# Kernel optimization log

Hardware: AMD Instinct MI355X
Metric: run time of the kernel (lower is better)

## Reference

```python
import jax, jax.numpy as jnp
import numpy as np

N, C_IN, C_RED, H, W = 16, 256, 64, 48, 48


def conv1x1(x, w, b):
    # x: [N, Cin, H, W], w: [Cout, Cin], b: [Cout]
    return jnp.einsum('nchw,oc->nohw', x, w) + b[None, :, None, None]


def setup_inputs() -> dict:
    key = jax.random.key(0)
    ks = jax.random.split(key, 10)
    s_in = 1.0 / np.sqrt(C_IN)
    s_red = 1.0 / np.sqrt(C_RED)
    return {
        'feature_maps': jax.random.normal(ks[0], (N, C_IN, H, W), jnp.float32),
        'global_channel_output': jax.random.normal(ks[1], (N, C_IN, H, W), jnp.float32),
        'Wq': jax.random.uniform(ks[2], (C_RED, C_IN), jnp.float32, -s_in, s_in),
        'bq': jax.random.uniform(ks[3], (C_RED,), jnp.float32, -s_in, s_in),
        'Wk': jax.random.uniform(ks[4], (C_RED, C_IN), jnp.float32, -s_in, s_in),
        'bk': jax.random.uniform(ks[5], (C_RED,), jnp.float32, -s_in, s_in),
        'Wv': jax.random.uniform(ks[6], (C_RED, C_IN), jnp.float32, -s_in, s_in),
        'bv': jax.random.uniform(ks[7], (C_RED,), jnp.float32, -s_in, s_in),
        'Watt': jax.random.uniform(ks[8], (C_IN, C_RED), jnp.float32, -s_red, s_red),
        'batt': jax.random.uniform(ks[9], (C_IN,), jnp.float32, -s_red, s_red),
    }


def reference(feature_maps, global_channel_output, Wq, bq, Wk, bk, Wv, bv, Watt, batt):
    n, _, h, w = feature_maps.shape
    hw = h * w
    q = conv1x1(feature_maps, Wq, bq).reshape(n, -1, hw)   # [N, Cr, HW]
    k = conv1x1(feature_maps, Wk, bk).reshape(n, -1, hw)   # [N, Cr, HW]
    v = conv1x1(feature_maps, Wv, bv).reshape(n, -1, hw)   # [N, Cr, HW]
    # key^T @ query -> [N, HW, HW]
    qk = jnp.einsum('nci,ncj->nij', k, q)
    # global (flattened) softmax over the whole HWxHW matrix per batch element
    qk = jax.nn.softmax(qk.reshape(n, hw * hw), axis=-1).reshape(n, hw, hw)
    att = jnp.einsum('nci,nij->ncj', v, qk).reshape(n, -1, h, w)  # [N, Cr, H, W]
    att = conv1x1(att, Watt, batt)                                 # [N, Cin, H, W]
    return global_channel_output * att + global_channel_output
```

## Files before the change

### kernel.cpp

```cpp
#include <hip/hip_runtime.h>
#include <hip/hip_bf16.h>
#include <stdint.h>

#define NB   16
#define CIN  256
#define CRED 64
#define HW   2304
#define NJT  36

typedef __bf16 bf16;
typedef __bf16 bf16x8 __attribute__((ext_vector_type(8)));
typedef __bf16 bf16x4 __attribute__((ext_vector_type(4)));
typedef float  f32x4  __attribute__((ext_vector_type(4)));

__global__ __launch_bounds__(256) void qkv_kernel(
    const float* __restrict__ x,
    const float* __restrict__ Wq, const float* __restrict__ bq,
    const float* __restrict__ Wk, const float* __restrict__ bk,
    const float* __restrict__ Wv, const float* __restrict__ bv,
    bf16* __restrict__ qT, bf16* __restrict__ kT, bf16* __restrict__ v)
{
    __shared__ __align__(16) bf16 sX[64 * 264];
    const int jt = blockIdx.x, n = blockIdx.y;
    const int jbase = jt * 64;
    const int tid = threadIdx.x;
    const int lane = tid & 63, w = tid >> 6;
    const int l15 = lane & 15, q4 = lane >> 4;

    const float* xn = x + ((size_t)n * CIN) * HW + jbase;
    #pragma unroll
    for (int it = 0; it < 16; ++it) {
        int idx = tid + 256 * it;
        int c = idx >> 4, p4 = idx & 15;
        const float4 vv = *(const float4*)(xn + c * HW + p4 * 4);
        sX[(p4 * 4 + 0) * 264 + c] = (bf16)vv.x;
        sX[(p4 * 4 + 1) * 264 + c] = (bf16)vv.y;
        sX[(p4 * 4 + 2) * 264 + c] = (bf16)vv.z;
        sX[(p4 * 4 + 3) * 264 + c] = (bf16)vv.w;
    }
    __syncthreads();

    const float* Ws[3] = {Wq, Wk, Wv};
    const float* bs[3] = {bq, bk, bv};
    #pragma unroll
    for (int wi = 0; wi < 3; ++wi) {
        bf16x8 a[8];
        const float* Wp = Ws[wi] + (w * 16 + l15) * CIN + q4 * 8;
        #pragma unroll
        for (int ks = 0; ks < 8; ++ks) {
            float4 f0 = *(const float4*)(Wp + ks * 32);
            float4 f1 = *(const float4*)(Wp + ks * 32 + 4);
            bf16x8 t = {(bf16)f0.x, (bf16)f0.y, (bf16)f0.z, (bf16)f0.w,
                        (bf16)f1.x, (bf16)f1.y, (bf16)f1.z, (bf16)f1.w};
            a[ks] = t;
        }
        f32x4 acc[4] = {};
        #pragma unroll
        for (int nt = 0; nt < 4; ++nt) {
            #pragma unroll
            for (int ks = 0; ks < 8; ++ks) {
                bf16x8 b = *(const bf16x8*)(sX + (nt * 16 + l15) * 264 + ks * 32 + q4 * 8);
                acc[nt] = __builtin_amdgcn_mfma_f32_16x16x32_bf16(a[ks], b, acc[nt], 0, 0, 0);
            }
        }
        const int crb = w * 16 + q4 * 4;
        const float b0 = bs[wi][crb], b1 = bs[wi][crb + 1],
                    b2 = bs[wi][crb + 2], b3 = bs[wi][crb + 3];
        if (wi < 2) {
            bf16* dst = (wi == 0 ? qT : kT) + ((size_t)n * HW) * 64;
            #pragma unroll
            for (int nt = 0; nt < 4; ++nt) {
                int pos = jbase + nt * 16 + l15;
                bf16x4 pk = {(bf16)(acc[nt].x + b0), (bf16)(acc[nt].y + b1),
                             (bf16)(acc[nt].z + b2), (bf16)(acc[nt].w + b3)};
                *(bf16x4*)(dst + pos * 64 + crb) = pk;
            }
        } else {
            bf16* dst = v + ((size_t)n * CRED) * HW;
            #pragma unroll
            for (int nt = 0; nt < 4; ++nt) {
                int pos = jbase + nt * 16 + l15;
                dst[(crb + 0) * HW + pos] = (bf16)(acc[nt].x + b0);
                dst[(crb + 1) * HW + pos] = (bf16)(acc[nt].y + b1);
                dst[(crb + 2) * HW + pos] = (bf16)(acc[nt].z + b2);
                dst[(crb + 3) * HW + pos] = (bf16)(acc[nt].w + b3);
            }
        }
    }
}

__global__ __launch_bounds__(256) void attn_kernel(
    const bf16* __restrict__ qT, const bf16* __restrict__ kT,
    const bf16* __restrict__ v,
    float* __restrict__ OT, float* __restrict__ Z)
{
    __shared__ __align__(16) bf16 sQ[64 * 72];
    __shared__ __align__(16) bf16 sK[64 * 72];
    __shared__ __align__(16) bf16 sV[64 * 72];
    __shared__ __align__(16) bf16 sP[64 * 72];
    const int jt = blockIdx.x, n = blockIdx.y;
    const int jbase = jt * 64;
    const int tid = threadIdx.x;
    const int lane = tid & 63, w = tid >> 6;
    const int l15 = lane & 15, q4 = lane >> 4;

    {
        const uint4* src = (const uint4*)(qT + ((size_t)n * HW + jbase) * 64);
        uint4* dst = (uint4*)sQ;
        for (int i = tid; i < 512; i += 256) {
            int r = i >> 3, c = i & 7;
            dst[r * 9 + c] = src[r * 8 + c];
        }
    }
    f32x4 oacc[4] = {};
    float zacc = 0.f;
    const uint4* ksrc = (const uint4*)(kT + ((size_t)n * HW) * 64);
    const bf16* vbase = v + ((size_t)n * CRED) * HW;

    for (int ib = 0; ib < NJT; ++ib) {
        const int ibase = ib * 64;
        __syncthreads();
        {
            uint4* dk = (uint4*)sK;
            uint4* dv = (uint4*)sV;
            const uint4* sk = ksrc + ibase * 8;
            for (int i = tid; i < 512; i += 256) {
                int r = i >> 3, c = i & 7;
                dk[r * 9 + c] = sk[r * 8 + c];
                dv[r * 9 + c] = *(const uint4*)(vbase + r * HW + ibase + c * 8);
            }
        }
        __syncthreads();
        f32x4 s[4];
        #pragma unroll
        for (int nt = 0; nt < 4; ++nt) {
            f32x4 accs = {};
            #pragma unroll
            for (int ks = 0; ks < 2; ++ks) {
                bf16x8 afr = *(const bf16x8*)(sK + (w * 16 + l15) * 72 + ks * 32 + q4 * 8);
                bf16x8 bfr = *(const bf16x8*)(sQ + (nt * 16 + l15) * 72 + ks * 32 + q4 * 8);
                accs = __builtin_amdgcn_mfma_f32_16x16x32_bf16(afr, bfr, accs, 0, 0, 0);
            }
            s[nt] = accs;
        }
        #pragma unroll
        for (int nt = 0; nt < 4; ++nt) {
            float p0 = __expf(s[nt].x), p1 = __expf(s[nt].y);
            float p2 = __expf(s[nt].z), p3 = __expf(s[nt].w);
            zacc += (p0 + p1) + (p2 + p3);
            bf16x4 pk = {(bf16)p0, (bf16)p1, (bf16)p2, (bf16)p3};
            *(bf16x4*)(sP + (nt * 16 + l15) * 72 + w * 16 + q4 * 4) = pk;
        }
        __syncthreads();
        #pragma unroll
        for (int nt = 0; nt < 4; ++nt) {
            #pragma unroll
            for (int ks = 0; ks < 2; ++ks) {
                bf16x8 afr = *(const bf16x8*)(sV + (w * 16 + l15) * 72 + ks * 32 + q4 * 8);
                bf16x8 bfr = *(const bf16x8*)(sP + (nt * 16 + l15) * 72 + ks * 32 + q4 * 8);
                oacc[nt] = __builtin_amdgcn_mfma_f32_16x16x32_bf16(afr, bfr, oacc[nt], 0, 0, 0);
            }
        }
    }
    float* OTn = OT + ((size_t)n * HW) * 64;
    #pragma unroll
    for (int nt = 0; nt < 4; ++nt) {
        int pos = jbase + nt * 16 + l15;
        *(f32x4*)(OTn + pos * 64 + w * 16 + q4 * 4) = oacc[nt];
    }
    #pragma unroll
    for (int off = 32; off > 0; off >>= 1) zacc += __shfl_down(zacc, off);
    if (lane == 0) atomicAdd(Z + n, zacc);
}

__global__ __launch_bounds__(256) void out_kernel(
    const float* __restrict__ OT, const float* __restrict__ Z,
    const float* __restrict__ Watt, const float* __restrict__ batt,
    const float* __restrict__ g, float* __restrict__ out)
{
    __shared__ __align__(16) bf16 sO[64 * 72];
    const int jt = blockIdx.x, n = blockIdx.y;
    const int jbase = jt * 64;
    const int tid = threadIdx.x;
    const int lane = tid & 63, w = tid >> 6;
    const int l15 = lane & 15, q4 = lane >> 4;
    const float invZ = 1.0f / Z[n];

    const float* On = OT + ((size_t)n * HW + jbase) * 64;
    for (int i = tid; i < 1024; i += 256) {
        int r = i >> 4, c4 = i & 15;
        float4 vv = *(const float4*)(On + r * 64 + c4 * 4);
        bf16x4 pk = {(bf16)(vv.x * invZ), (bf16)(vv.y * invZ),
                     (bf16)(vv.z * invZ), (bf16)(vv.w * invZ)};
        *(bf16x4*)(sO + r * 72 + c4 * 4) = pk;
    }
    __syncthreads();

    bf16x8 a[4][2];
    #pragma unroll
    for (int mt = 0; mt < 4; ++mt) {
        const float* Wp = Watt + (w * 64 + mt * 16 + l15) * 64 + q4 * 8;
        #pragma unroll
        for (int ks = 0; ks < 2; ++ks) {
            float4 f0 = *(const float4*)(Wp + ks * 32);
            float4 f1 = *(const float4*)(Wp + ks * 32 + 4);
            bf16x8 t = {(bf16)f0.x, (bf16)f0.y, (bf16)f0.z, (bf16)f0.w,
                        (bf16)f1.x, (bf16)f1.y, (bf16)f1.z, (bf16)f1.w};
            a[mt][ks] = t;
        }
    }
    const float* gp = g + ((size_t)n * CIN) * HW;
    float* op = out + ((size_t)n * CIN) * HW;
    #pragma unroll
    for (int mt = 0; mt < 4; ++mt) {
        #pragma unroll
        for (int nt = 0; nt < 4; ++nt) {
            f32x4 acc = {};
            #pragma unroll
            for (int ks = 0; ks < 2; ++ks) {
                bf16x8 b = *(const bf16x8*)(sO + (nt * 16 + l15) * 72 + ks * 32 + q4 * 8);
                acc = __builtin_amdgcn_mfma_f32_16x16x32_bf16(a[mt][ks], b, acc, 0, 0, 0);
            }
            const int co = w * 64 + mt * 16 + q4 * 4;
            const int pos = jbase + nt * 16 + l15;
            const float b0 = batt[co], b1 = batt[co + 1], b2 = batt[co + 2], b3 = batt[co + 3];
            const float g0 = gp[(co + 0) * HW + pos], g1 = gp[(co + 1) * HW + pos];
            const float g2 = gp[(co + 2) * HW + pos], g3 = gp[(co + 3) * HW + pos];
            op[(co + 0) * HW + pos] = g0 * (acc.x + b0 + 1.0f);
            op[(co + 1) * HW + pos] = g1 * (acc.y + b1 + 1.0f);
            op[(co + 2) * HW + pos] = g2 * (acc.z + b2 + 1.0f);
            op[(co + 3) * HW + pos] = g3 * (acc.w + b3 + 1.0f);
        }
    }
}

extern "C" void kernel_launch(void* const* d_in, const int* in_sizes, int n_in,
                              void* d_out, int out_size, void* d_ws, size_t ws_size,
                              hipStream_t stream) {
    const float* x    = (const float*)d_in[0];
    const float* g    = (const float*)d_in[1];
    const float* Wq   = (const float*)d_in[2];
    const float* bq   = (const float*)d_in[3];
    const float* Wk   = (const float*)d_in[4];
    const float* bk   = (const float*)d_in[5];
    const float* Wv   = (const float*)d_in[6];
    const float* bv   = (const float*)d_in[7];
    const float* Watt = (const float*)d_in[8];
    const float* batt = (const float*)d_in[9];
    float* out = (float*)d_out;

    char* ws = (char*)d_ws;
    const size_t qkv_sz = (size_t)NB * HW * CRED * sizeof(bf16);
    bf16*  qT = (bf16*)(ws);
    bf16*  kT = (bf16*)(ws + qkv_sz);
    bf16*  vv = (bf16*)(ws + 2 * qkv_sz);
    float* OT = (float*)(ws + 3 * qkv_sz);
    float* Z  = (float*)(ws + 3 * qkv_sz + (size_t)NB * HW * CRED * sizeof(float));

    hipMemsetAsync(Z, 0, NB * sizeof(float), stream);

    dim3 grid(NJT, NB), blk(256);
    qkv_kernel<<<grid, blk, 0, stream>>>(x, Wq, bq, Wk, bk, Wv, bv, qT, kT, vv);
    attn_kernel<<<grid, blk, 0, stream>>>(qT, kT, vv, OT, Z);
    out_kernel<<<grid, blk, 0, stream>>>(OT, Z, Watt, batt, g, out);
}
```

Baseline: 255.0 us.

## Split attention key range across blocks and reduce partials in output kernel

```diff
diff --git a/kernel.cpp b/kernel.cpp
--- a/kernel.cpp
+++ b/kernel.cpp
@@ -7,6 +7,8 @@
 #define CRED 64
 #define HW   2304
 #define NJT  36
+#define NIG  4
+#define NIT  9
 
 typedef __bf16 bf16;
 typedef __bf16 bf16x8 __attribute__((ext_vector_type(8)));
@@ -92,13 +94,13 @@
 __global__ __launch_bounds__(256) void attn_kernel(
     const bf16* __restrict__ qT, const bf16* __restrict__ kT,
     const bf16* __restrict__ v,
-    float* __restrict__ OT, float* __restrict__ Z)
+    float* __restrict__ OTp, float* __restrict__ Z)
 {
     __shared__ __align__(16) bf16 sQ[64 * 72];
     __shared__ __align__(16) bf16 sK[64 * 72];
     __shared__ __align__(16) bf16 sV[64 * 72];
     __shared__ __align__(16) bf16 sP[64 * 72];
-    const int jt = blockIdx.x, n = blockIdx.y;
+    const int jt = blockIdx.x, ig = blockIdx.y, n = blockIdx.z;
     const int jbase = jt * 64;
     const int tid = threadIdx.x;
     const int lane = tid & 63, w = tid >> 6;
@@ -112,13 +114,21 @@
             dst[r * 9 + c] = src[r * 8 + c];
         }
     }
+    __syncthreads();
+    bf16x8 qf[4][2];
+    #pragma unroll
+    for (int nt = 0; nt < 4; ++nt)
+        #pragma unroll
+        for (int ks = 0; ks < 2; ++ks)
+            qf[nt][ks] = *(const bf16x8*)(sQ + (nt * 16 + l15) * 72 + ks * 32 + q4 * 8);
+
     f32x4 oacc[4] = {};
     float zacc = 0.f;
     const uint4* ksrc = (const uint4*)(kT + ((size_t)n * HW) * 64);
     const bf16* vbase = v + ((size_t)n * CRED) * HW;
 
-    for (int ib = 0; ib < NJT; ++ib) {
-        const int ibase = ib * 64;
+    for (int it = 0; it < NIT; ++it) {
+        const int ibase = (ig * NIT + it) * 64;
         __syncthreads();
         {
             uint4* dk = (uint4*)sK;
@@ -131,38 +141,31 @@
             }
         }
         __syncthreads();
-        f32x4 s[4];
+        bf16x8 kf0 = *(const bf16x8*)(sK + (w * 16 + l15) * 72 + 0 * 32 + q4 * 8);
+        bf16x8 kf1 = *(const bf16x8*)(sK + (w * 16 + l15) * 72 + 1 * 32 + q4 * 8);
         #pragma unroll
         for (int nt = 0; nt < 4; ++nt) {
             f32x4 accs = {};
-            #pragma unroll
-            for (int ks = 0; ks < 2; ++ks) {
-                bf16x8 afr = *(const bf16x8*)(sK + (w * 16 + l15) * 72 + ks * 32 + q4 * 8);
-                bf16x8 bfr = *(const bf16x8*)(sQ + (nt * 16 + l15) * 72 + ks * 32 + q4 * 8);
-                accs = __builtin_amdgcn_mfma_f32_16x16x32_bf16(afr, bfr, accs, 0, 0, 0);
-            }
-            s[nt] = accs;
-        }
-        #pragma unroll
-        for (int nt = 0; nt < 4; ++nt) {
-            float p0 = __expf(s[nt].x), p1 = __expf(s[nt].y);
-            float p2 = __expf(s[nt].z), p3 = __expf(s[nt].w);
+            accs = __builtin_amdgcn_mfma_f32_16x16x32_bf16(kf0, qf[nt][0], accs, 0, 0, 0);
+            accs = __builtin_amdgcn_mfma_f32_16x16x32_bf16(kf1, qf[nt][1], accs, 0, 0, 0);
+            float p0 = __expf(accs.x), p1 = __expf(accs.y);
+            float p2 = __expf(accs.z), p3 = __expf(accs.w);
             zacc += (p0 + p1) + (p2 + p3);
             bf16x4 pk = {(bf16)p0, (bf16)p1, (bf16)p2, (bf16)p3};
             *(bf16x4*)(sP + (nt * 16 + l15) * 72 + w * 16 + q4 * 4) = pk;
         }
         __syncthreads();
+        bf16x8 vf0 = *(const bf16x8*)(sV + (w * 16 + l15) * 72 + 0 * 32 + q4 * 8);
+        bf16x8 vf1 = *(const bf16x8*)(sV + (w * 16 + l15) * 72 + 1 * 32 + q4 * 8);
         #pragma unroll
         for (int nt = 0; nt < 4; ++nt) {
-            #pragma unroll
-            for (int ks = 0; ks < 2; ++ks) {
-                bf16x8 afr = *(const bf16x8*)(sV + (w * 16 + l15) * 72 + ks * 32 + q4 * 8);
-                bf16x8 bfr = *(const bf16x8*)(sP + (nt * 16 + l15) * 72 + ks * 32 + q4 * 8);
-                oacc[nt] = __builtin_amdgcn_mfma_f32_16x16x32_bf16(afr, bfr, oacc[nt], 0, 0, 0);
-            }
-        }
-    }
-    float* OTn = OT + ((size_t)n * HW) * 64;
+            bf16x8 p0 = *(const bf16x8*)(sP + (nt * 16 + l15) * 72 + 0 * 32 + q4 * 8);
+            bf16x8 p1 = *(const bf16x8*)(sP + (nt * 16 + l15) * 72 + 1 * 32 + q4 * 8);
+            oacc[nt] = __builtin_amdgcn_mfma_f32_16x16x32_bf16(vf0, p0, oacc[nt], 0, 0, 0);
+            oacc[nt] = __builtin_amdgcn_mfma_f32_16x16x32_bf16(vf1, p1, oacc[nt], 0, 0, 0);
+        }
+    }
+    float* OTn = OTp + (((size_t)ig * NB + n) * HW) * 64;
     #pragma unroll
     for (int nt = 0; nt < 4; ++nt) {
         int pos = jbase + nt * 16 + l15;
@@ -174,63 +177,60 @@
 }
 
 __global__ __launch_bounds__(256) void out_kernel(
-    const float* __restrict__ OT, const float* __restrict__ Z,
+    const float* __restrict__ OTp, const float* __restrict__ Z,
     const float* __restrict__ Watt, const float* __restrict__ batt,
     const float* __restrict__ g, float* __restrict__ out)
 {
-    __shared__ __align__(16) bf16 sO[64 * 72];
+    __shared__ __align__(16) bf16 sO[16 * 72];
     const int jt = blockIdx.x, n = blockIdx.y;
-    const int jbase = jt * 64;
+    const int jbase = jt * 16;
     const int tid = threadIdx.x;
     const int lane = tid & 63, w = tid >> 6;
     const int l15 = lane & 15, q4 = lane >> 4;
     const float invZ = 1.0f / Z[n];
 
-    const float* On = OT + ((size_t)n * HW + jbase) * 64;
-    for (int i = tid; i < 1024; i += 256) {
-        int r = i >> 4, c4 = i & 15;
-        float4 vv = *(const float4*)(On + r * 64 + c4 * 4);
-        bf16x4 pk = {(bf16)(vv.x * invZ), (bf16)(vv.y * invZ),
-                     (bf16)(vv.z * invZ), (bf16)(vv.w * invZ)};
+    {
+        int r = tid >> 4, c4 = tid & 15;
+        const float* p = OTp + (((size_t)n * HW) + jbase + r) * 64 + c4 * 4;
+        float4 v0 = *(const float4*)(p);
+        float4 v1 = *(const float4*)(p + (size_t)NB * HW * 64);
+        float4 v2 = *(const float4*)(p + 2 * (size_t)NB * HW * 64);
+        float4 v3 = *(const float4*)(p + 3 * (size_t)NB * HW * 64);
+        bf16x4 pk = {(bf16)((v0.x + v1.x + v2.x + v3.x) * invZ),
+                     (bf16)((v0.y + v1.y + v2.y + v3.y) * invZ),
+                     (bf16)((v0.z + v1.z + v2.z + v3.z) * invZ),
+                     (bf16)((v0.w + v1.w + v2.w + v3.w) * invZ)};
         *(bf16x4*)(sO + r * 72 + c4 * 4) = pk;
     }
     __syncthreads();
 
-    bf16x8 a[4][2];
+    const float* gp = g + ((size_t)n * CIN) * HW;
+    float* op = out + ((size_t)n * CIN) * HW;
+    bf16x8 b0 = *(const bf16x8*)(sO + l15 * 72 + 0 * 32 + q4 * 8);
+    bf16x8 b1 = *(const bf16x8*)(sO + l15 * 72 + 1 * 32 + q4 * 8);
     #pragma unroll
     for (int mt = 0; mt < 4; ++mt) {
         const float* Wp = Watt + (w * 64 + mt * 16 + l15) * 64 + q4 * 8;
-        #pragma unroll
-        for (int ks = 0; ks < 2; ++ks) {
-            float4 f0 = *(const float4*)(Wp + ks * 32);
-            float4 f1 = *(const float4*)(Wp + ks * 32 + 4);
-            bf16x8 t = {(bf16)f0.x, (bf16)f0.y, (bf16)f0.z, (bf16)f0.w,
-                        (bf16)f1.x, (bf16)f1.y, (bf16)f1.z, (bf16)f1.w};
-            a[mt][ks] = t;
-        }
-    }
-    const float* gp = g + ((size_t)n * CIN) * HW;
-    float* op = out + ((size_t)n * CIN) * HW;
-    #pragma unroll
-    for (int mt = 0; mt < 4; ++mt) {
-        #pragma unroll
-        for (int nt = 0; nt < 4; ++nt) {
-            f32x4 acc = {};
-            #pragma unroll
-            for (int ks = 0; ks < 2; ++ks) {
-                bf16x8 b = *(const bf16x8*)(sO + (nt * 16 + l15) * 72 + ks * 32 + q4 * 8);
-                acc = __builtin_amdgcn_mfma_f32_16x16x32_bf16(a[mt][ks], b, acc, 0, 0, 0);
-            }
-            const int co = w * 64 + mt * 16 + q4 * 4;
-            const int pos = jbase + nt * 16 + l15;
-            const float b0 = batt[co], b1 = batt[co + 1], b2 = batt[co + 2], b3 = batt[co + 3];
-            const float g0 = gp[(co + 0) * HW + pos], g1 = gp[(co + 1) * HW + pos];
-            const float g2 = gp[(co + 2) * HW + pos], g3 = gp[(co + 3) * HW + pos];
-            op[(co + 0) * HW + pos] = g0 * (acc.x + b0 + 1.0f);
-            op[(co + 1) * HW + pos] = g1 * (acc.y + b1 + 1.0f);
-            op[(co + 2) * HW + pos] = g2 * (acc.z + b2 + 1.0f);
-            op[(co + 3) * HW + pos] = g3 * (acc.w + b3 + 1.0f);
-        }
+        float4 f0 = *(const float4*)(Wp);
+        float4 f1 = *(const float4*)(Wp + 4);
+        float4 f2 = *(const float4*)(Wp + 32);
+        float4 f3 = *(const float4*)(Wp + 36);
+        bf16x8 a0 = {(bf16)f0.x, (bf16)f0.y, (bf16)f0.z, (bf16)f0.w,
+                     (bf16)f1.x, (bf16)f1.y, (bf16)f1.z, (bf16)f1.w};
+        bf16x8 a1 = {(bf16)f2.x, (bf16)f2.y, (bf16)f2.z, (bf16)f2.w,
+                     (bf16)f3.x, (bf16)f3.y, (bf16)f3.z, (bf16)f3.w};
+        f32x4 acc = {};
+        acc = __builtin_amdgcn_mfma_f32_16x16x32_bf16(a0, b0, acc, 0, 0, 0);
+        acc = __builtin_amdgcn_mfma_f32_16x16x32_bf16(a1, b1, acc, 0, 0, 0);
+        const int co = w * 64 + mt * 16 + q4 * 4;
+        const int pos = jbase + l15;
+        const float c0 = batt[co], c1 = batt[co + 1], c2 = batt[co + 2], c3 = batt[co + 3];
+        const float g0 = gp[(co + 0) * HW + pos], g1 = gp[(co + 1) * HW + pos];
+        const float g2 = gp[(co + 2) * HW + pos], g3 = gp[(co + 3) * HW + pos];
+        op[(co + 0) * HW + pos] = g0 * (acc.x + c0 + 1.0f);
+        op[(co + 1) * HW + pos] = g1 * (acc.y + c1 + 1.0f);
+        op[(co + 2) * HW + pos] = g2 * (acc.z + c2 + 1.0f);
+        op[(co + 3) * HW + pos] = g3 * (acc.w + c3 + 1.0f);
     }
 }
 
@@ -254,13 +254,13 @@
     bf16*  qT = (bf16*)(ws);
     bf16*  kT = (bf16*)(ws + qkv_sz);
     bf16*  vv = (bf16*)(ws + 2 * qkv_sz);
-    float* OT = (float*)(ws + 3 * qkv_sz);
-    float* Z  = (float*)(ws + 3 * qkv_sz + (size_t)NB * HW * CRED * sizeof(float));
+    float* OTp = (float*)(ws + 3 * qkv_sz);
+    float* Z  = (float*)(ws + 3 * qkv_sz + (size_t)NIG * NB * HW * CRED * sizeof(float));
 
     hipMemsetAsync(Z, 0, NB * sizeof(float), stream);
 
-    dim3 grid(NJT, NB), blk(256);
-    qkv_kernel<<<grid, blk, 0, stream>>>(x, Wq, bq, Wk, bk, Wv, bv, qT, kT, vv);
-    attn_kernel<<<grid, blk, 0, stream>>>(qT, kT, vv, OT, Z);
-    out_kernel<<<grid, blk, 0, stream>>>(OT, Z, Watt, batt, g, out);
-}
+    dim3 blk(256);
+    qkv_kernel<<<dim3(NJT, NB), blk, 0, stream>>>(x, Wq, bq, Wk, bk, Wv, bv, qT, kT, vv);
+    attn_kernel<<<dim3(NJT, NIG, NB), blk, 0, stream>>>(qT, kT, vv, OTp, Z);
+    out_kernel<<<dim3(HW / 16, NB), blk, 0, stream>>>(OTp, Z, Watt, batt, g, out);
+}
```

New measurement: 329.1 us. 29.0% more time.
